# Kernel optimization log

Measured on AMD Instinct MI355X. Metric: run time of the kernel, lower is better.

The kernel has to match this reference:

```python
import jax, jax.numpy as jnp
import numpy as np

COLOR_SIZE = 4
SIZE = 64
FILTERS = 512
LENGTH = SIZE * SIZE * 3  # 12288


def setup_inputs() -> dict:
    key = jax.random.key(0)
    k1, k2, k3 = jax.random.split(key, 3)
    example = jax.random.randint(k1, (8, SIZE, SIZE, 3), 0, COLOR_SIZE, dtype=jnp.int32)
    kernel = jax.random.normal(k2, (FILTERS, LENGTH), dtype=jnp.float32)
    bias = jnp.zeros((FILTERS,), dtype=jnp.float32)
    dense_w = jax.random.normal(k3, (FILTERS, COLOR_SIZE), dtype=jnp.float32) * 0.02
    dense_b = jnp.zeros((COLOR_SIZE,), dtype=jnp.float32)
    return {"example": example, "kernel": kernel, "bias": bias,
            "dense_w": dense_w, "dense_b": dense_b}


def reference(example, kernel, bias, dense_w, dense_b):
    B = example.shape[0]
    L = kernel.shape[1]  # 12288
    # normalize int pixels to [-1, 1)
    x = example.astype(jnp.float32) / COLOR_SIZE * 2.0 - 1.0
    x = x.reshape(B, L)                                   # [B, L]
    # FFT-based long (causal full) convolution, fft_length = 2L
    Xf = jnp.fft.rfft(x, n=2 * L, axis=-1)                # [B, L+1] complex64
    Kf = jnp.fft.rfft(kernel, n=2 * L, axis=-1)           # [F, L+1]
    y = jnp.fft.irfft(Xf[:, None, :] * Kf[None, :, :], n=2 * L, axis=-1)[..., :L]  # [B, F, L]
    y = jnp.transpose(y, (0, 2, 1)) + bias                # [B, L, F]
    y = jax.nn.relu(y)
    out = y @ dense_w + dense_b                           # [B, L, color_size]
    return out.reshape(B, SIZE, SIZE, 3, COLOR_SIZE).astype(jnp.float32)
```

## Files before the change

kernel.cpp:

```cpp
#include <hip/hip_runtime.h>

#define FF 512
#define LL 12288
#define NJC 1556
#define NR 128

typedef _Float16 half8 __attribute__((ext_vector_type(8)));
typedef float    f32x16 __attribute__((ext_vector_type(16)));

__global__ __launch_bounds__(256) void build_At(const float* __restrict__ kern,
                                                _Float16* __restrict__ At) {
    int tid  = blockIdx.x * 256 + threadIdx.x;
    int lane = tid & 63;
    int rest = tid >> 6;
    int kc   = rest % 768;
    int fgt  = rest / 768;
    int f    = fgt * 32 + (lane & 31);
    int d0   = kc * 16 + (lane >> 5) * 8;
    const float* src = kern + (size_t)f * LL + d0;
    half8 v;
#pragma unroll
    for (int i = 0; i < 8; ++i) v[i] = (_Float16)src[i];
    ((half8*)At)[tid] = v;
}

__global__ __launch_bounds__(256) void build_XB(const int* __restrict__ ex,
                                                _Float16* __restrict__ XB) {
    int tid = blockIdx.x * 256 + threadIdx.x;
    if (tid >= NJC * NR) return;
    int r  = tid & 127;
    int jc = tid >> 7;
    int s  = r >> 3, b = r & 7;
    int j0 = jc * 8;
    half8 v;
#pragma unroll
    for (int i = 0; i < 8; ++i) {
        int idx = LL - 1 - (j0 + i) - s;
        float x = 0.f;
        if (idx >= 0) x = (float)ex[b * LL + idx] * 0.5f - 1.0f;
        v[i] = (_Float16)x;
    }
    ((half8*)XB)[tid] = v;
}

__global__ __launch_bounds__(256) void init_out(const float* __restrict__ db,
                                                float* __restrict__ out) {
    int tid = blockIdx.x * 256 + threadIdx.x;
    out[tid] = db[tid & 3];
}

__device__ __forceinline__ void gl_lds16(const half8* g, half8* l) {
    __builtin_amdgcn_global_load_lds((const __attribute__((address_space(1))) void*)g,
                                     (__attribute__((address_space(3))) void*)l, 16, 0, 0);
}

__global__ __launch_bounds__(256, 2) void conv_main(const _Float16* __restrict__ At,
                                                    const _Float16* __restrict__ XB,
                                                    const float* __restrict__ bias,
                                                    const float* __restrict__ dw,
                                                    float* __restrict__ out) {
    __shared__ half8 Abuf[2][8][4][64];

    int bx    = blockIdx.x;
    int slot  = bx & 7;
    int f_blk = slot >> 1;
    int n_blk = 383 - ((bx >> 3) * 2 + (slot & 1));
    int n0 = n_blk << 5;
    int M  = (n_blk + 4) >> 2;

    int tid  = threadIdx.x;
    int lane = tid & 63;
    int wid  = tid >> 6;
    int wf   = wid >> 1;
    int wc   = wid & 1;
    int bb   = lane & 7;
    int nq   = (lane >> 3) & 3;
    int kh   = lane >> 5;

    const half8* Ag = (const half8*)At;
    const half8* ag[8];
#pragma unroll
    for (int u = 0; u < 8; ++u) {
        int kcl = wid * 2 + (u >> 2);
        int ft  = u & 3;
        ag[u] = Ag + ((size_t)(f_blk * 4 + ft) * 768 + kcl) * 64 + lane;
    }

    const half8* Bg = (const half8*)XB;
    const half8* pB[4];
#pragma unroll
    for (int cf = 0; cf < 4; ++cf) {
        int n  = n0 + wc * 16 + cf * 4 + nq;
        int T  = LL - 1 - n + 8 * kh;
        pB[cf] = Bg + (size_t)(T >> 3) * 128 + (T & 7) * 8 + bb;
    }

    f32x16 acc[2][4];
#pragma unroll
    for (int rf = 0; rf < 2; ++rf)
#pragma unroll
        for (int cf = 0; cf < 4; ++cf)
#pragma unroll
            for (int i = 0; i < 16; ++i) acc[rf][cf][i] = 0.f;

#pragma unroll
    for (int u = 0; u < 8; ++u)
        gl_lds16(ag[u], &Abuf[0][wid * 2 + (u >> 2)][u & 3][lane]);
    half8 bcur[4], bnxt[4];
#pragma unroll
    for (int cf = 0; cf < 4; ++cf) bcur[cf] = pB[cf][0];
#pragma unroll
    for (int cf = 0; cf < 4; ++cf) pB[cf] += 256;
    __syncthreads();

    for (int mc = 0; mc < M; ++mc) {
        int buf = mc & 1;
        if (mc + 1 < M) {
            size_t oa = (size_t)(mc + 1) * 512;
#pragma unroll
            for (int u = 0; u < 8; ++u)
                gl_lds16(ag[u] + oa, &Abuf[buf ^ 1][wid * 2 + (u >> 2)][u & 3][lane]);
        }
#pragma unroll
        for (int kc = 0; kc < 8; ++kc) {
#pragma unroll
            for (int cf = 0; cf < 4; ++cf) bnxt[cf] = pB[cf][0];
#pragma unroll
            for (int cf = 0; cf < 4; ++cf) pB[cf] += 256;
            half8 a0 = Abuf[buf][kc][wf * 2 + 0][lane];
            half8 a1 = Abuf[buf][kc][wf * 2 + 1][lane];
#pragma unroll
            for (int cf = 0; cf < 4; ++cf)
                acc[0][cf] = __builtin_amdgcn_mfma_f32_32x32x16_f16(a0, bcur[cf], acc[0][cf], 0, 0, 0);
#pragma unroll
            for (int cf = 0; cf < 4; ++cf)
                acc[1][cf] = __builtin_amdgcn_mfma_f32_32x32x16_f16(a1, bcur[cf], acc[1][cf], 0, 0, 0);
#pragma unroll
            for (int cf = 0; cf < 4; ++cf) bcur[cf] = bnxt[cf];
        }
        __syncthreads();
    }

    float p[4][4];
#pragma unroll
    for (int cf = 0; cf < 4; ++cf)
#pragma unroll
        for (int c = 0; c < 4; ++c) p[cf][c] = 0.f;

#pragma unroll
    for (int rf = 0; rf < 2; ++rf) {
#pragma unroll
        for (int reg = 0; reg < 16; ++reg) {
            int f = f_blk * 128 + wf * 64 + rf * 32 + (reg & 3) + 8 * (reg >> 2) + 4 * kh;
            float bs = bias[f];
            float4 w = *(const float4*)(dw + (size_t)f * 4);
#pragma unroll
            for (int cf = 0; cf < 4; ++cf) {
                float y = fmaxf(acc[rf][cf][reg] + bs, 0.f);
                p[cf][0] += y * w.x; p[cf][1] += y * w.y;
                p[cf][2] += y * w.z; p[cf][3] += y * w.w;
            }
        }
    }
#pragma unroll
    for (int cf = 0; cf < 4; ++cf)
#pragma unroll
        for (int c = 0; c < 4; ++c)
            p[cf][c] += __shfl_xor(p[cf][c], 32, 64);
    if (kh == 0) {
#pragma unroll
        for (int cf = 0; cf < 4; ++cf) {
            int n = n0 + wc * 16 + cf * 4 + nq;
            float* o = out + ((size_t)bb * LL + n) * 4;
#pragma unroll
            for (int c = 0; c < 4; ++c) atomicAdd(o + c, p[cf][c]);
        }
    }
}

extern "C" void kernel_launch(void* const* d_in, const int* in_sizes, int n_in,
                              void* d_out, int out_size, void* d_ws, size_t ws_size,
                              hipStream_t stream) {
    const int*   ex   = (const int*)d_in[0];
    const float* kern = (const float*)d_in[1];
    const float* bias = (const float*)d_in[2];
    const float* dw   = (const float*)d_in[3];
    const float* db   = (const float*)d_in[4];
    float* out = (float*)d_out;

    _Float16* At = (_Float16*)d_ws;
    _Float16* XB = (_Float16*)((char*)d_ws + (size_t)FF * LL * 2);

    hipLaunchKernelGGL(build_At, dim3(3072), dim3(256), 0, stream, kern, At);
    hipLaunchKernelGGL(build_XB, dim3(778),  dim3(256), 0, stream, ex, XB);
    hipLaunchKernelGGL(init_out, dim3(1536), dim3(256), 0, stream, db, out);
    hipLaunchKernelGGL(conv_main, dim3(1536), dim3(256), 0, stream, At, XB, bias, dw, out);
}
```

Measured before the change: 562.9 us.

## Re-tile warps to cover all filters with fewer columns, deepen B prefetch

Each warp now computes all four 32-filter row fragments against two 4-column B fragments, instead of two row fragments against four column fragments. The warp tiling moves from a 2x2 filter-by-column split to a split over columns only. This halves per-warp global B loads at the cost of doubling LDS reads of A per k-step. It also adds a second register stage to the B prefetch, loading two steps ahead to hide global latency better, which needs slightly more registers.

```diff
diff --git a/kernel.cpp b/kernel.cpp
--- a/kernel.cpp
+++ b/kernel.cpp
@@ -71,8 +71,6 @@
     int tid  = threadIdx.x;
     int lane = tid & 63;
     int wid  = tid >> 6;
-    int wf   = wid >> 1;
-    int wc   = wid & 1;
     int bb   = lane & 7;
     int nq   = (lane >> 3) & 3;
     int kh   = lane >> 5;
@@ -87,30 +85,32 @@
     }
 
     const half8* Bg = (const half8*)XB;
-    const half8* pB[4];
+    const half8* pB[2];
 #pragma unroll
-    for (int cf = 0; cf < 4; ++cf) {
-        int n  = n0 + wc * 16 + cf * 4 + nq;
+    for (int cf = 0; cf < 2; ++cf) {
+        int n  = n0 + wid * 8 + cf * 4 + nq;
         int T  = LL - 1 - n + 8 * kh;
         pB[cf] = Bg + (size_t)(T >> 3) * 128 + (T & 7) * 8 + bb;
     }
 
-    f32x16 acc[2][4];
+    f32x16 acc[4][2];
 #pragma unroll
-    for (int rf = 0; rf < 2; ++rf)
+    for (int rf = 0; rf < 4; ++rf)
 #pragma unroll
-        for (int cf = 0; cf < 4; ++cf)
+        for (int cf = 0; cf < 2; ++cf)
 #pragma unroll
             for (int i = 0; i < 16; ++i) acc[rf][cf][i] = 0.f;
 
 #pragma unroll
     for (int u = 0; u < 8; ++u)
         gl_lds16(ag[u], &Abuf[0][wid * 2 + (u >> 2)][u & 3][lane]);
-    half8 bcur[4], bnxt[4];
+    half8 b0[2], b1[2], b2[2];
 #pragma unroll
-    for (int cf = 0; cf < 4; ++cf) bcur[cf] = pB[cf][0];
-#pragma unroll
-    for (int cf = 0; cf < 4; ++cf) pB[cf] += 256;
+    for (int cf = 0; cf < 2; ++cf) {
+        b0[cf] = pB[cf][0];
+        b1[cf] = pB[cf][256];
+        pB[cf] += 512;
+    }
     __syncthreads();
 
     for (int mc = 0; mc < M; ++mc) {
@@ -124,38 +124,36 @@
 #pragma unroll
         for (int kc = 0; kc < 8; ++kc) {
 #pragma unroll
-            for (int cf = 0; cf < 4; ++cf) bnxt[cf] = pB[cf][0];
+            for (int cf = 0; cf < 2; ++cf) { b2[cf] = pB[cf][0]; pB[cf] += 256; }
+            half8 a[4];
 #pragma unroll
-            for (int cf = 0; cf < 4; ++cf) pB[cf] += 256;
-            half8 a0 = Abuf[buf][kc][wf * 2 + 0][lane];
-            half8 a1 = Abuf[buf][kc][wf * 2 + 1][lane];
+            for (int rf = 0; rf < 4; ++rf) a[rf] = Abuf[buf][kc][rf][lane];
 #pragma unroll
-            for (int cf = 0; cf < 4; ++cf)
-                acc[0][cf] = __builtin_amdgcn_mfma_f32_32x32x16_f16(a0, bcur[cf], acc[0][cf], 0, 0, 0);
+            for (int rf = 0; rf < 4; ++rf)
 #pragma unroll
-            for (int cf = 0; cf < 4; ++cf)
-                acc[1][cf] = __builtin_amdgcn_mfma_f32_32x32x16_f16(a1, bcur[cf], acc[1][cf], 0, 0, 0);
+                for (int cf = 0; cf < 2; ++cf)
+                    acc[rf][cf] = __builtin_amdgcn_mfma_f32_32x32x16_f16(a[rf], b0[cf], acc[rf][cf], 0, 0, 0);
 #pragma unroll
-            for (int cf = 0; cf < 4; ++cf) bcur[cf] = bnxt[cf];
+            for (int cf = 0; cf < 2; ++cf) { b0[cf] = b1[cf]; b1[cf] = b2[cf]; }
         }
         __syncthreads();
     }
 
-    float p[4][4];
+    float p[2][4];
 #pragma unroll
-    for (int cf = 0; cf < 4; ++cf)
+    for (int cf = 0; cf < 2; ++cf)
 #pragma unroll
         for (int c = 0; c < 4; ++c) p[cf][c] = 0.f;
 
 #pragma unroll
-    for (int rf = 0; rf < 2; ++rf) {
+    for (int rf = 0; rf < 4; ++rf) {
 #pragma unroll
         for (int reg = 0; reg < 16; ++reg) {
-            int f = f_blk * 128 + wf * 64 + rf * 32 + (reg & 3) + 8 * (reg >> 2) + 4 * kh;
+            int f = f_blk * 128 + rf * 32 + (reg & 3) + 8 * (reg >> 2) + 4 * kh;
             float bs = bias[f];
             float4 w = *(const float4*)(dw + (size_t)f * 4);
 #pragma unroll
-            for (int cf = 0; cf < 4; ++cf) {
+            for (int cf = 0; cf < 2; ++cf) {
                 float y = fmaxf(acc[rf][cf][reg] + bs, 0.f);
                 p[cf][0] += y * w.x; p[cf][1] += y * w.y;
                 p[cf][2] += y * w.z; p[cf][3] += y * w.w;
@@ -163,14 +161,14 @@
         }
     }
 #pragma unroll
-    for (int cf = 0; cf < 4; ++cf)
+    for (int cf = 0; cf < 2; ++cf)
 #pragma unroll
         for (int c = 0; c < 4; ++c)
             p[cf][c] += __shfl_xor(p[cf][c], 32, 64);
     if (kh == 0) {
 #pragma unroll
-        for (int cf = 0; cf < 4; ++cf) {
-            int n = n0 + wc * 16 + cf * 4 + nq;
+        for (int cf = 0; cf < 2; ++cf) {
+            int n = n0 + wid * 8 + cf * 4 + nq;
             float* o = out + ((size_t)bb * LL + n) * 4;
 #pragma unroll
             for (int c = 0; c < 4; ++c) atomicAdd(o + c, p[cf][c]);
```

Result: faster. 534.5 us (-5.0%).
